# Optimization experiments

Hardware: AMD Instinct MI355X
Metric: run time of the kernel (lower is better)

## Reference

```python
import jax, jax.numpy as jnp
import numpy as np

B, T, D, H, L, F = 32, 512, 1024, 1024, 2, 256  # batch, time, input dim, units, layers, feature_size


def setup_inputs() -> dict:
    key = jax.random.key(0)
    ks = jax.random.split(key, 9)
    s_in = 1.0 / np.sqrt(D)
    s_h = 1.0 / np.sqrt(H)
    x = jax.random.normal(ks[0], (B, T, D), dtype=jnp.float32)
    # Stacked LSTM params: gate order [i, f, g, o] concatenated along last axis.
    Wx = jax.random.normal(ks[1], (L, D, 4 * H), dtype=jnp.float32) * s_in
    Wh = jax.random.normal(ks[2], (L, H, 4 * H), dtype=jnp.float32) * s_h
    b = jnp.zeros((L, 4 * H), dtype=jnp.float32)
    # Output heads.
    Wmu = jax.random.normal(ks[3], (H, F), dtype=jnp.float32) * s_h
    bmu = jnp.zeros((F,), dtype=jnp.float32)
    Wls = jax.random.normal(ks[4], (H, F), dtype=jnp.float32) * s_h
    bls = jnp.zeros((F,), dtype=jnp.float32)
    y_min = jnp.zeros((F,), dtype=jnp.float32)  # y_min init arg (0.0 broadcast)
    return {"x": x, "Wx": Wx, "Wh": Wh, "b": b, "Wmu": Wmu, "bmu": bmu,
            "Wls": Wls, "bls": bls, "y_min": y_min}


def _lstm_layer(x, Wx, Wh, b):
    # x: [B, T, Din]; Wx: [Din, 4H]; Wh: [H, 4H]; b: [4H]
    Bn = x.shape[0]
    Hn = Wh.shape[0]
    # Precompute input projections for all timesteps (one big GEMM).
    x_proj = jnp.einsum('btd,dg->btg', x, Wx) + b  # [B, T, 4H]

    def step(carry, xp):
        h, c = carry
        g = xp + h @ Wh  # [B, 4H]
        i, f, gg, o = jnp.split(g, 4, axis=-1)
        c = jax.nn.sigmoid(f) * c + jax.nn.sigmoid(i) * jnp.tanh(gg)
        h = jax.nn.sigmoid(o) * jnp.tanh(c)
        return (h, c), h

    h0 = jnp.zeros((Bn, Hn), dtype=x.dtype)
    c0 = jnp.zeros((Bn, Hn), dtype=x.dtype)
    _, hs = jax.lax.scan(step, (h0, c0), jnp.swapaxes(x_proj, 0, 1))  # hs: [T, B, H]
    return jnp.swapaxes(hs, 0, 1)  # [B, T, H]


def reference(x, Wx, Wh, b, Wmu, bmu, Wls, bls, y_min):
    for l in range(Wx.shape[0]):  # small fixed n_layers loop
        x = _lstm_layer(x, Wx[l], Wh[l], b[l])
    mu = jax.nn.softplus(x @ Wmu + bmu) + y_min  # [B, T, F]
    log_sigma = x @ Wls + bls                    # [B, T, F]
    return (mu, log_sigma)
```

## Files before the change

kernel.cpp:

```cpp
#include <hip/hip_runtime.h>

typedef unsigned short u16;
typedef unsigned int   u32;
typedef unsigned long long u64;
typedef short s16x4 __attribute__((ext_vector_type(4)));
typedef short s16x8 __attribute__((ext_vector_type(8)));
typedef float f32x4 __attribute__((ext_vector_type(4)));
typedef u32   u32x4 __attribute__((ext_vector_type(4)));

#define GK 1024

__device__ inline u16 f2bf(float f) {
    u32 u = __builtin_bit_cast(u32, f);
    u += 0x7FFFu + ((u >> 16) & 1u);
    return (u16)(u >> 16);
}
__device__ inline u16 f2h(float f) {
    _Float16 h = (_Float16)f;
    return __builtin_bit_cast(u16, h);
}
__device__ inline float h2f(u16 u) {
    return (float)__builtin_bit_cast(_Float16, u);
}
__device__ inline float fast_sigmoid(float x) {
    return __builtin_amdgcn_rcpf(1.f + __expf(-x));
}
__device__ inline float fast_tanh(float x) {
    return 1.f - 2.f * __builtin_amdgcn_rcpf(1.f + __expf(2.f * x));
}
__device__ inline f32x4 mfma16(s16x8 a, s16x8 b, f32x4 c) {
    return __builtin_amdgcn_mfma_f32_16x16x32_bf16(a, b, c, 0, 0, 0);
}
__device__ inline s16x8 mk8(s16x4 lo, s16x4 hi) {
    return __builtin_shufflevector(lo, hi, 0, 1, 2, 3, 4, 5, 6, 7);
}

__global__ void k_f2bf(const float* __restrict__ in, u16* __restrict__ out, int n) {
    int i = (blockIdx.x * 256 + threadIdx.x) * 4;
    if (i < n) {
        float4 v = *(const float4*)(in + i);
        ushort4 o;
        o.x = f2bf(v.x); o.y = f2bf(v.y); o.z = f2bf(v.z); o.w = f2bf(v.w);
        *(ushort4*)(out + i) = o;
    }
}

__global__ void k_transpose_bf(const float* __restrict__ in, u16* __restrict__ out,
                               int R, int C) {
    __shared__ float tile[32][33];
    int tid = threadIdx.x;
    int xs = (tid & 7) * 4;
    int y  = tid >> 3;
    int r0 = blockIdx.y * 32, c0 = blockIdx.x * 32;
    float4 v = *(const float4*)(in + (size_t)(r0 + y) * C + c0 + xs);
    tile[y][xs + 0] = v.x; tile[y][xs + 1] = v.y;
    tile[y][xs + 2] = v.z; tile[y][xs + 3] = v.w;
    __syncthreads();
    ushort4 o;
    o.x = f2bf(tile[xs + 0][y]); o.y = f2bf(tile[xs + 1][y]);
    o.z = f2bf(tile[xs + 2][y]); o.w = f2bf(tile[xs + 3][y]);
    *(ushort4*)(out + (size_t)(c0 + y) * R + r0 + xs) = o;
}

template<int MODE>
__launch_bounds__(256, 2)
__global__ void k_gemm(const u16* __restrict__ A, const u16* __restrict__ BT,
                       const float* __restrict__ bias,
                       u16* __restrict__ Cb, float* __restrict__ Cf,
                       const float* __restrict__ b2, const float* __restrict__ ymin,
                       int gridN) {
    int bid = blockIdx.x;
    int m0 = (bid / gridN) * 128, n0 = (bid % gridN) * 128;
    __shared__ u16 As[128 * 40];
    __shared__ u16 Bs[128 * 40];
    int tid = threadIdx.x;
    int lane = tid & 63, w = tid >> 6;
    int wr = w >> 1, wc = w & 1;
    int rr = lane & 15, r16 = lane >> 4;
    f32x4 acc[4][4] = {};
    for (int kt = 0; kt < GK / 32; ++kt) {
        int k0 = kt * 32;
#pragma unroll
        for (int it = 0; it < 2; ++it) {
            int idx = it * 256 + tid;
            int row = idx >> 2, ch = idx & 3;
            if (MODE == 0) {
                *(u32x4*)(&As[row * 40 + ch * 8]) =
                    *(const u32x4*)(A + (size_t)(m0 + row) * GK + k0 + ch * 8);
            } else {
                int m = m0 + row;
                size_t aaddr = (size_t)(m >> 5) * 32768 + (size_t)((k0 >> 3) + ch) * 256
                             + (size_t)(m & 31) * 8;
                *(u32x4*)(&As[row * 40 + ch * 8]) = *(const u32x4*)(A + aaddr);
            }
            *(u32x4*)(&Bs[row * 40 + ch * 8]) =
                *(const u32x4*)(BT + (size_t)(n0 + row) * GK + k0 + ch * 8);
        }
        __syncthreads();
        s16x8 af[4], bfr[4];
#pragma unroll
        for (int i = 0; i < 4; ++i) {
            int abase = (wr * 64 + i * 16 + rr) * 40 + r16 * 4;
            af[i] = mk8(*(const s16x4*)(&As[abase]), *(const s16x4*)(&As[abase + 16]));
            int bbase = (wc * 64 + i * 16 + rr) * 40 + r16 * 4;
            bfr[i] = mk8(*(const s16x4*)(&Bs[bbase]), *(const s16x4*)(&Bs[bbase + 16]));
        }
#pragma unroll
        for (int i = 0; i < 4; ++i)
#pragma unroll
            for (int j = 0; j < 4; ++j)
                acc[i][j] = mfma16(af[i], bfr[j], acc[i][j]);
        __syncthreads();
    }
#pragma unroll
    for (int i = 0; i < 4; ++i) {
#pragma unroll
        for (int j = 0; j < 4; ++j) {
#pragma unroll
            for (int r = 0; r < 4; ++r) {
                int m = m0 + wr * 64 + i * 16 + r16 * 4 + r;
                int n = n0 + wc * 64 + j * 16 + rr;
                float v = acc[i][j][r];
                if (MODE == 0) {
                    v += bias[n];
                    int orow = (m & 511) * 32 + (m >> 9);
                    int colx = ((n & 1023) << 2) | (n >> 10);
                    Cb[(size_t)orow * 4096 + colx] = f2h(v);
                } else {
                    int orow = (m & 31) * 512 + (m >> 5);
                    if (n < 256) {
                        v += bias[n];
                        float sp = fmaxf(v, 0.f) + log1pf(expf(-fabsf(v)));
                        Cf[(size_t)orow * 256 + n] = sp + ymin[n];
                    } else {
                        v += b2[n - 256];
                        Cf[4194304 + (size_t)orow * 256 + (n - 256)] = v;
                    }
                }
            }
        }
    }
}

__launch_bounds__(512, 2)
__global__ void k_fused(const u16* __restrict__ Wh0T, const u16* __restrict__ Wx1T,
                        const u16* __restrict__ Wh1T, const u16* __restrict__ xproj,
                        const float* __restrict__ b1,
                        u16* __restrict__ hseq0, u16* __restrict__ hseq1,
                        u32* __restrict__ flags) {
    __shared__ u16 wlds[2][32][128][8];
    __shared__ float part[4][64][4];
    int tid = threadIdx.x, blk = blockIdx.x;
    int lane = tid & 63, w = tid >> 6;
    int grp = w >> 2, wl = w & 3;
    int mt = wl >> 1, nt = wl & 1;
    int u0 = blk * 8;
    int rr = lane & 15, r16 = lane >> 4;

    int cg = (rr & 3) * 1024 + u0 + nt * 4 + (rr >> 2);
    if (wl < 2) {
        const u16* wsrc = (grp == 0 ? Wh0T : Wh1T) + (size_t)cg * GK + r16 * 4;
#pragma unroll
        for (int q = 0; q < 32; ++q) {
            s16x8 f = mk8(*(const s16x4*)(wsrc + q * 32),
                          *(const s16x4*)(wsrc + q * 32 + 16));
            *(s16x8*)(&wlds[grp][q][nt * 64 + lane][0]) = f;
        }
    }
    u64 wpx_u = (u64)(uintptr_t)(Wx1T + (size_t)cg * GK + r16 * 4);

    int b_    = mt * 16 + (lane >> 4) * 4 + (lane & 3);
    int u_loc = nt * 4 + ((lane >> 2) & 3);
    int unit  = u0 + u_loc;
    float c0 = 0.f, c1 = 0.f;
    float b1r[4];
#pragma unroll
    for (int g = 0; g < 4; ++g) b1r[g] = b1[g * 1024 + unit];

    const u16* xp = xproj + (size_t)b_ * 4096 + (size_t)unit * 4;
    const int boff = (mt * 16 + rr) * 8 + (r16 & 1) * 4;
    const int kq   = (r16 >> 1);
    const int soff = blk * 256 + b_ * 8 + nt * 4;
    const u16* wq = &wlds[grp][0][nt * 64 + lane][0];

    __syncthreads();

    for (int r = 0; r <= 512; ++r) {
        if (w == 0) {
            u32 tgt = (u32)r;
            while (true) {
                u32 v0 = __hip_atomic_load(&flags[lane], __ATOMIC_RELAXED,
                                           __HIP_MEMORY_SCOPE_AGENT);
                u32 v1 = __hip_atomic_load(&flags[64 + lane], __ATOMIC_RELAXED,
                                           __HIP_MEMORY_SCOPE_AGENT);
                if (__all((v0 >= tgt) & (v1 >= tgt))) break;
                __builtin_amdgcn_s_sleep(1);
            }
        }
        __syncthreads();

        f32x4 aE = {}, aO = {}, xE = {}, xO = {};
        u64 xv = 0;
        if (grp == 0) {
            if (r < 512) xv = *(const u64*)(xp + (size_t)r * 131072);
            asm volatile("" : "+v"(wpx_u));
            const u16* wpx = (const u16*)(uintptr_t)wpx_u;
            const u16* h0p = hseq0 + (size_t)r * 32768 + boff;
#pragma unroll
            for (int c = 0; c < 4; ++c) {
                u64 lo8[8], hi8[8];
                s16x8 bx[8];
#pragma unroll
                for (int j = 0; j < 8; ++j) {
                    int q = c * 8 + j;
                    lo8[j] = __hip_atomic_load((const u64*)(h0p + (q * 4 + kq) * 256),
                                               __ATOMIC_RELAXED, __HIP_MEMORY_SCOPE_AGENT);
                    hi8[j] = __hip_atomic_load((const u64*)(h0p + (q * 4 + kq + 2) * 256),
                                               __ATOMIC_RELAXED, __HIP_MEMORY_SCOPE_AGENT);
                    bx[j] = mk8(*(const s16x4*)(wpx + q * 32),
                                *(const s16x4*)(wpx + q * 32 + 16));
                }
#pragma unroll
                for (int j = 0; j < 8; ++j) {
                    int q = c * 8 + j;
                    s16x8 a = mk8(__builtin_bit_cast(s16x4, lo8[j]),
                                  __builtin_bit_cast(s16x4, hi8[j]));
                    s16x8 bw = *(const s16x8*)(wq + (size_t)q * 1024);
                    if (q & 1) { aO = mfma16(a, bw, aO); xO = mfma16(a, bx[j], xO); }
                    else       { aE = mfma16(a, bw, aE); xE = mfma16(a, bx[j], xE); }
                }
            }
        } else {
            if (r > 0) {
                const u16* h1p = hseq1 + (size_t)(r - 1) * 32768 + boff;
#pragma unroll
                for (int c = 0; c < 4; ++c) {
                    u64 lo8[8], hi8[8];
#pragma unroll
                    for (int j = 0; j < 8; ++j) {
                        int q = c * 8 + j;
                        lo8[j] = __hip_atomic_load((const u64*)(h1p + (q * 4 + kq) * 256),
                                                   __ATOMIC_RELAXED, __HIP_MEMORY_SCOPE_AGENT);
                        hi8[j] = __hip_atomic_load((const u64*)(h1p + (q * 4 + kq + 2) * 256),
                                                   __ATOMIC_RELAXED, __HIP_MEMORY_SCOPE_AGENT);
                    }
#pragma unroll
                    for (int j = 0; j < 8; ++j) {
                        int q = c * 8 + j;
                        s16x8 a = mk8(__builtin_bit_cast(s16x4, lo8[j]),
                                      __builtin_bit_cast(s16x4, hi8[j]));
                        s16x8 bw = *(const s16x8*)(wq + (size_t)q * 1024);
                        if (q & 1) aO = mfma16(a, bw, aO);
                        else       aE = mfma16(a, bw, aE);
                    }
                }
            }
            *(f32x4*)(&part[wl][lane][0]) = aE + aO;
        }
        __syncthreads();

        if (grp == 0) {
            if (r < 512) {
                f32x4 acc = aE + aO;
                float r0 = acc[0], r1 = acc[1], r2 = acc[2], r3 = acc[3];
                float x0 = __shfl_xor(r0, 1), x1 = __shfl_xor(r1, 1);
                float x2 = __shfl_xor(r2, 1), x3 = __shfl_xor(r3, 1);
                bool o1 = lane & 1;
                float s0 = o1 ? x1 : r0, s1 = o1 ? r1 : x0;
                float s2 = o1 ? x3 : r2, s3 = o1 ? r3 : x2;
                float y0 = __shfl_xor(s0, 2), y1 = __shfl_xor(s1, 2);
                float y2 = __shfl_xor(s2, 2), y3 = __shfl_xor(s3, 2);
                bool o2 = lane & 2;
                float gi = (o2 ? y2 : s0) + h2f((u16)(xv));
                float gf = (o2 ? y3 : s1) + h2f((u16)(xv >> 16));
                float gg = (o2 ? s2 : y0) + h2f((u16)(xv >> 32));
                float go = (o2 ? s3 : y1) + h2f((u16)(xv >> 48));
                float I  = fast_sigmoid(gi);
                float Fg = fast_sigmoid(gf);
                float G  = fast_tanh(gg);
                float O  = fast_sigmoid(go);
                c0 = Fg * c0 + I * G;
                u32 hq = (u32)f2bf(O * fast_tanh(c0));
                u32 o4 = (u32)__shfl_xor((int)hq, 4);
                u32 m32 = (lane & 4) ? ((o4 & 0xffffu) | (hq << 16))
                                     : ((hq & 0xffffu) | (o4 << 16));
                u32 o8 = (u32)__shfl_xor((int)m32, 8);
                u64 m64 = (lane & 8) ? (((u64)o8) | ((u64)m32 << 32))
                                     : (((u64)m32) | ((u64)o8 << 32));
                if ((lane & 12) == 0)
                    __hip_atomic_store((u64*)(hseq0 + (size_t)(r + 1) * 32768 + soff),
                                       m64, __ATOMIC_RELAXED, __HIP_MEMORY_SCOPE_AGENT);
            }
            if (r > 0) {
                f32x4 acc = xE + xO + *(const f32x4*)(&part[wl][lane][0]);
                float r0 = acc[0], r1 = acc[1], r2 = acc[2], r3 = acc[3];
                float x0 = __shfl_xor(r0, 1), x1 = __shfl_xor(r1, 1);
                float x2 = __shfl_xor(r2, 1), x3 = __shfl_xor(r3, 1);
                bool o1 = lane & 1;
                float s0 = o1 ? x1 : r0, s1 = o1 ? r1 : x0;
                float s2 = o1 ? x3 : r2, s3 = o1 ? r3 : x2;
                float y0 = __shfl_xor(s0, 2), y1 = __shfl_xor(s1, 2);
                float y2 = __shfl_xor(s2, 2), y3 = __shfl_xor(s3, 2);
                bool o2 = lane & 2;
                float gi = (o2 ? y2 : s0) + b1r[0];
                float gf = (o2 ? y3 : s1) + b1r[1];
                float gg = (o2 ? s2 : y0) + b1r[2];
                float go = (o2 ? s3 : y1) + b1r[3];
                float I  = fast_sigmoid(gi);
                float Fg = fast_sigmoid(gf);
                float G  = fast_tanh(gg);
                float O  = fast_sigmoid(go);
                c1 = Fg * c1 + I * G;
                u32 hq = (u32)f2bf(O * fast_tanh(c1));
                u32 o4 = (u32)__shfl_xor((int)hq, 4);
                u32 m32 = (lane & 4) ? ((o4 & 0xffffu) | (hq << 16))
                                     : ((hq & 0xffffu) | (o4 << 16));
                u32 o8 = (u32)__shfl_xor((int)m32, 8);
                u64 m64 = (lane & 8) ? (((u64)o8) | ((u64)m32 << 32))
                                     : (((u64)m32) | ((u64)o8 << 32));
                if ((lane & 12) == 0)
                    __hip_atomic_store((u64*)(hseq1 + (size_t)r * 32768 + soff),
                                       m64, __ATOMIC_RELAXED, __HIP_MEMORY_SCOPE_AGENT);
            }
        }
        __syncthreads();
        if (tid == 0)
            __hip_atomic_store(&flags[blk], (u32)(r + 1), __ATOMIC_RELAXED,
                               __HIP_MEMORY_SCOPE_AGENT);
    }
}

extern "C" void kernel_launch(void* const* d_in, const int* in_sizes, int n_in,
                              void* d_out, int out_size, void* d_ws, size_t ws_size,
                              hipStream_t stream) {
    const float* x   = (const float*)d_in[0];
    const float* Wx  = (const float*)d_in[1];
    const float* Wh  = (const float*)d_in[2];
    const float* b   = (const float*)d_in[3];
    const float* Wmu = (const float*)d_in[4];
    const float* bmu = (const float*)d_in[5];
    const float* Wls = (const float*)d_in[6];
    const float* bls = (const float*)d_in[7];
    const float* ym  = (const float*)d_in[8];
    float* out = (float*)d_out;

    char* ws = (char*)d_ws;
    u16* hseq0 = (u16*)(ws);
    u16* xbf   = (u16*)(ws);
    u16* hseq1 = (u16*)(ws + 33619968);
    u16* wxT   = (u16*)(ws + 67239936);
    u16* whT   = (u16*)(ws + 84017152);
    u16* whdT  = (u16*)(ws + 100794368);
    u16* xproj = (u16*)(ws + 101842944);
    u32* flags = (u32*)(ws + 236060672);

    k_f2bf<<<16384, 256, 0, stream>>>(x, xbf, 16777216);
    dim3 tg(128, 32);
    k_transpose_bf<<<tg, 256, 0, stream>>>(Wx,           wxT,           1024, 4096);
    k_transpose_bf<<<tg, 256, 0, stream>>>(Wx + 4194304, wxT + 4194304, 1024, 4096);
    k_transpose_bf<<<tg, 256, 0, stream>>>(Wh,           whT,           1024, 4096);
    k_transpose_bf<<<tg, 256, 0, stream>>>(Wh + 4194304, whT + 4194304, 1024, 4096);
    dim3 hg(8, 32);
    k_transpose_bf<<<hg, 256, 0, stream>>>(Wmu, whdT,          1024, 256);
    k_transpose_bf<<<hg, 256, 0, stream>>>(Wls, whdT + 262144, 1024, 256);

    k_gemm<0><<<4096, 256, 0, stream>>>(xbf, wxT, b, xproj, nullptr, nullptr, nullptr, 32);

    hipMemsetAsync(hseq0, 0, 65536, stream);
    hipMemsetAsync(hseq1, 0, 65536, stream);
    hipMemsetAsync(flags, 0, 512, stream);

    k_fused<<<128, 512, 0, stream>>>(whT, wxT + 4194304, whT + 4194304, xproj,
                                     b + 4096, hseq0, hseq1, flags);

    k_gemm<1><<<512, 256, 0, stream>>>(hseq1 + 32768, whdT, bmu, nullptr, out,
                                       bls, ym, 4);
}
```

Measured before the change: 8.023 ms.

## Split recurrent K across wave pairs and relayout hidden-state exchange buffers

Reorganizes the fused recurrent LSTM kernel so each wave pair splits the K dimension in halves and covers both N tiles, reducing partial sums through shared memory. The hidden-state sequence buffer layout changes to a contiguous per-K-chunk format, so loads become two adjacent 8-byte atomics instead of strided ones. A new unpack kernel converts the layer-1 hidden states to row-major before the head GEMM, which then drops its special addressing path. Occupancy hint is lowered to one block per CU. The aim is to shorten the per-timestep critical path, at the cost of an extra unpack pass and more LDS reduction traffic.

```diff
diff --git a/kernel.cpp b/kernel.cpp
--- a/kernel.cpp
+++ b/kernel.cpp
@@ -33,6 +33,9 @@
 }
 __device__ inline s16x8 mk8(s16x4 lo, s16x4 hi) {
     return __builtin_shufflevector(lo, hi, 0, 1, 2, 3, 4, 5, 6, 7);
+}
+__device__ inline u64 ald(const u16* p) {
+    return __hip_atomic_load((const u64*)p, __ATOMIC_RELAXED, __HIP_MEMORY_SCOPE_AGENT);
 }
 
 __global__ void k_f2bf(const float* __restrict__ in, u16* __restrict__ out, int n) {
@@ -60,6 +63,19 @@
     o.x = f2bf(tile[xs + 0][y]); o.y = f2bf(tile[xs + 1][y]);
     o.z = f2bf(tile[xs + 2][y]); o.w = f2bf(tile[xs + 3][y]);
     *(ushort4*)(out + (size_t)(c0 + y) * R + r0 + xs) = o;
+}
+
+__global__ void k_unpack(const u16* __restrict__ in, u16* __restrict__ out) {
+    int idx = blockIdx.x * 256 + threadIdx.x;
+    int slot = idx >> 12;
+    int c = idx & 4095;
+    int q = c >> 7, b = (c >> 2) & 31, ri = c & 3;
+    const u16* p = in + (size_t)(slot + 1) * 32768 + q * 1024 + b * 32 + ri * 8;
+    u64 lo = *(const u64*)p;
+    u64 hi = *(const u64*)(p + 4);
+    u16* o = out + (size_t)(slot * 32 + b) * 1024 + q * 32 + ri * 4;
+    *(u64*)o = lo;
+    *(u64*)(o + 16) = hi;
 }
 
 template<int MODE>
@@ -84,15 +100,8 @@
         for (int it = 0; it < 2; ++it) {
             int idx = it * 256 + tid;
             int row = idx >> 2, ch = idx & 3;
-            if (MODE == 0) {
-                *(u32x4*)(&As[row * 40 + ch * 8]) =
-                    *(const u32x4*)(A + (size_t)(m0 + row) * GK + k0 + ch * 8);
-            } else {
-                int m = m0 + row;
-                size_t aaddr = (size_t)(m >> 5) * 32768 + (size_t)((k0 >> 3) + ch) * 256
-                             + (size_t)(m & 31) * 8;
-                *(u32x4*)(&As[row * 40 + ch * 8]) = *(const u32x4*)(A + aaddr);
-            }
+            *(u32x4*)(&As[row * 40 + ch * 8]) =
+                *(const u32x4*)(A + (size_t)(m0 + row) * GK + k0 + ch * 8);
             *(u32x4*)(&Bs[row * 40 + ch * 8]) =
                 *(const u32x4*)(BT + (size_t)(n0 + row) * GK + k0 + ch * 8);
         }
@@ -142,46 +151,46 @@
     }
 }
 
-__launch_bounds__(512, 2)
+__launch_bounds__(512, 1)
 __global__ void k_fused(const u16* __restrict__ Wh0T, const u16* __restrict__ Wx1T,
                         const u16* __restrict__ Wh1T, const u16* __restrict__ xproj,
                         const float* __restrict__ b1,
                         u16* __restrict__ hseq0, u16* __restrict__ hseq1,
                         u32* __restrict__ flags) {
-    __shared__ u16 wlds[2][32][128][8];
-    __shared__ float part[4][64][4];
+    __shared__ u16 wlds[2][32][2][64][8];
+    __shared__ f32x4 part[2][2][4][64];
     int tid = threadIdx.x, blk = blockIdx.x;
     int lane = tid & 63, w = tid >> 6;
     int grp = w >> 2, wl = w & 3;
-    int mt = wl >> 1, nt = wl & 1;
+    int mt = wl >> 1, qh = wl & 1;
     int u0 = blk * 8;
     int rr = lane & 15, r16 = lane >> 4;
 
-    int cg = (rr & 3) * 1024 + u0 + nt * 4 + (rr >> 2);
     if (wl < 2) {
+        int ntp = wl;
+        int cg = (rr & 3) * 1024 + u0 + ntp * 4 + (rr >> 2);
         const u16* wsrc = (grp == 0 ? Wh0T : Wh1T) + (size_t)cg * GK + r16 * 4;
 #pragma unroll
         for (int q = 0; q < 32; ++q) {
-            s16x8 f = mk8(*(const s16x4*)(wsrc + q * 32),
-                          *(const s16x4*)(wsrc + q * 32 + 16));
-            *(s16x8*)(&wlds[grp][q][nt * 64 + lane][0]) = f;
-        }
-    }
-    u64 wpx_u = (u64)(uintptr_t)(Wx1T + (size_t)cg * GK + r16 * 4);
-
-    int b_    = mt * 16 + (lane >> 4) * 4 + (lane & 3);
-    int u_loc = nt * 4 + ((lane >> 2) & 3);
-    int unit  = u0 + u_loc;
+            *(s16x8*)(&wlds[grp][q][ntp][lane][0]) =
+                mk8(*(const s16x4*)(wsrc + q * 32), *(const s16x4*)(wsrc + q * 32 + 16));
+        }
+    }
+    u64 wpx_u = (u64)(uintptr_t)(Wx1T +
+        (size_t)((rr & 3) * 1024 + u0 + (rr >> 2)) * GK + r16 * 4);
+
+    int b_ = mt * 16 + (lane >> 4) * 4 + (lane & 3);
+    int uu = (lane >> 2) & 3;
+    int unit = u0 + qh * 4 + uu;
     float c0 = 0.f, c1 = 0.f;
     float b1r[4];
 #pragma unroll
     for (int g = 0; g < 4; ++g) b1r[g] = b1[g * 1024 + unit];
-
     const u16* xp = xproj + (size_t)b_ * 4096 + (size_t)unit * 4;
-    const int boff = (mt * 16 + rr) * 8 + (r16 & 1) * 4;
-    const int kq   = (r16 >> 1);
-    const int soff = blk * 256 + b_ * 8 + nt * 4;
-    const u16* wq = &wlds[grp][0][nt * 64 + lane][0];
+
+    int sblk = blk & 3;
+    const int soff = (blk >> 2) * 1024 + b_ * 32 + (((sblk & 1) * 2 + qh) * 8 + (sblk >> 1) * 4);
+    const int cbase = qh * 16384 + mt * 512 + rr * 32 + r16 * 8;
 
     __syncthreads();
 
@@ -198,70 +207,73 @@
             }
         }
         __syncthreads();
-
-        f32x4 aE = {}, aO = {}, xE = {}, xO = {};
+        __builtin_amdgcn_sched_barrier(0);
+
+        f32x4 a0[2] = {}, a1[2] = {};
         u64 xv = 0;
         if (grp == 0) {
             if (r < 512) xv = *(const u64*)(xp + (size_t)r * 131072);
             asm volatile("" : "+v"(wpx_u));
             const u16* wpx = (const u16*)(uintptr_t)wpx_u;
-            const u16* h0p = hseq0 + (size_t)r * 32768 + boff;
+            const u16* hp = hseq0 + (size_t)r * 32768 + cbase;
 #pragma unroll
             for (int c = 0; c < 4; ++c) {
-                u64 lo8[8], hi8[8];
-                s16x8 bx[8];
-#pragma unroll
-                for (int j = 0; j < 8; ++j) {
-                    int q = c * 8 + j;
-                    lo8[j] = __hip_atomic_load((const u64*)(h0p + (q * 4 + kq) * 256),
-                                               __ATOMIC_RELAXED, __HIP_MEMORY_SCOPE_AGENT);
-                    hi8[j] = __hip_atomic_load((const u64*)(h0p + (q * 4 + kq + 2) * 256),
-                                               __ATOMIC_RELAXED, __HIP_MEMORY_SCOPE_AGENT);
-                    bx[j] = mk8(*(const s16x4*)(wpx + q * 32),
-                                *(const s16x4*)(wpx + q * 32 + 16));
+                u64 lo4[4], hi4[4];
+                s16x8 bx0[4], bx1[4];
+#pragma unroll
+                for (int j = 0; j < 4; ++j) {
+                    int jj = c * 4 + j;
+                    int q = qh * 16 + jj;
+                    lo4[j] = ald(hp + jj * 1024);
+                    hi4[j] = ald(hp + jj * 1024 + 4);
+                    const u16* bp = wpx + q * 32;
+                    bx0[j] = mk8(*(const s16x4*)bp, *(const s16x4*)(bp + 16));
+                    bx1[j] = mk8(*(const s16x4*)(bp + 4096),
+                                 *(const s16x4*)(bp + 4096 + 16));
                 }
 #pragma unroll
-                for (int j = 0; j < 8; ++j) {
-                    int q = c * 8 + j;
-                    s16x8 a = mk8(__builtin_bit_cast(s16x4, lo8[j]),
-                                  __builtin_bit_cast(s16x4, hi8[j]));
-                    s16x8 bw = *(const s16x8*)(wq + (size_t)q * 1024);
-                    if (q & 1) { aO = mfma16(a, bw, aO); xO = mfma16(a, bx[j], xO); }
-                    else       { aE = mfma16(a, bw, aE); xE = mfma16(a, bx[j], xE); }
+                for (int j = 0; j < 4; ++j) {
+                    int q = qh * 16 + c * 4 + j;
+                    s16x8 a = mk8(__builtin_bit_cast(s16x4, lo4[j]),
+                                  __builtin_bit_cast(s16x4, hi4[j]));
+                    a0[0] = mfma16(a, *(const s16x8*)(&wlds[0][q][0][lane][0]), a0[0]);
+                    a0[1] = mfma16(a, *(const s16x8*)(&wlds[0][q][1][lane][0]), a0[1]);
+                    a1[0] = mfma16(a, bx0[j], a1[0]);
+                    a1[1] = mfma16(a, bx1[j], a1[1]);
                 }
             }
+            part[mt][1 - qh][0][lane] = a0[1 - qh];
+            part[mt][1 - qh][1][lane] = a1[1 - qh];
         } else {
             if (r > 0) {
-                const u16* h1p = hseq1 + (size_t)(r - 1) * 32768 + boff;
+                const u16* hp = hseq1 + (size_t)(r - 1) * 32768 + cbase;
 #pragma unroll
                 for (int c = 0; c < 4; ++c) {
-                    u64 lo8[8], hi8[8];
-#pragma unroll
-                    for (int j = 0; j < 8; ++j) {
-                        int q = c * 8 + j;
-                        lo8[j] = __hip_atomic_load((const u64*)(h1p + (q * 4 + kq) * 256),
-                                                   __ATOMIC_RELAXED, __HIP_MEMORY_SCOPE_AGENT);
-                        hi8[j] = __hip_atomic_load((const u64*)(h1p + (q * 4 + kq + 2) * 256),
-                                                   __ATOMIC_RELAXED, __HIP_MEMORY_SCOPE_AGENT);
+                    u64 lo4[4], hi4[4];
+#pragma unroll
+                    for (int j = 0; j < 4; ++j) {
+                        int jj = c * 4 + j;
+                        lo4[j] = ald(hp + jj * 1024);
+                        hi4[j] = ald(hp + jj * 1024 + 4);
                     }
 #pragma unroll
-                    for (int j = 0; j < 8; ++j) {
-                        int q = c * 8 + j;
-                        s16x8 a = mk8(__builtin_bit_cast(s16x4, lo8[j]),
-                                      __builtin_bit_cast(s16x4, hi8[j]));
-                        s16x8 bw = *(const s16x8*)(wq + (size_t)q * 1024);
-                        if (q & 1) aO = mfma16(a, bw, aO);
-                        else       aE = mfma16(a, bw, aE);
+                    for (int j = 0; j < 4; ++j) {
+                        int q = qh * 16 + c * 4 + j;
+                        s16x8 a = mk8(__builtin_bit_cast(s16x4, lo4[j]),
+                                      __builtin_bit_cast(s16x4, hi4[j]));
+                        a0[0] = mfma16(a, *(const s16x8*)(&wlds[1][q][0][lane][0]), a0[0]);
+                        a0[1] = mfma16(a, *(const s16x8*)(&wlds[1][q][1][lane][0]), a0[1]);
                     }
                 }
             }
-            *(f32x4*)(&part[wl][lane][0]) = aE + aO;
+            part[mt][0][2 + qh][lane] = a0[0];
+            part[mt][1][2 + qh][lane] = a0[1];
         }
         __syncthreads();
 
         if (grp == 0) {
             if (r < 512) {
-                f32x4 acc = aE + aO;
+                f32x4 acc = a0[qh] + part[mt][qh][0][lane];
                 float r0 = acc[0], r1 = acc[1], r2 = acc[2], r3 = acc[3];
                 float x0 = __shfl_xor(r0, 1), x1 = __shfl_xor(r1, 1);
                 float x2 = __shfl_xor(r2, 1), x3 = __shfl_xor(r3, 1);
@@ -292,7 +304,8 @@
                                        m64, __ATOMIC_RELAXED, __HIP_MEMORY_SCOPE_AGENT);
             }
             if (r > 0) {
-                f32x4 acc = xE + xO + *(const f32x4*)(&part[wl][lane][0]);
+                f32x4 acc = a1[qh] + part[mt][qh][1][lane]
+                          + part[mt][qh][2][lane] + part[mt][qh][3][lane];
                 float r0 = acc[0], r1 = acc[1], r2 = acc[2], r3 = acc[3];
                 float x0 = __shfl_xor(r0, 1), x1 = __shfl_xor(r1, 1);
                 float x2 = __shfl_xor(r2, 1), x3 = __shfl_xor(r3, 1);
@@ -352,6 +365,7 @@
     u16* whT   = (u16*)(ws + 84017152);
     u16* whdT  = (u16*)(ws + 100794368);
     u16* xproj = (u16*)(ws + 101842944);
+    u16* h1lin = xproj;
     u32* flags = (u32*)(ws + 236060672);
 
     k_f2bf<<<16384, 256, 0, stream>>>(x, xbf, 16777216);
@@ -373,6 +387,6 @@
     k_fused<<<128, 512, 0, stream>>>(whT, wxT + 4194304, whT + 4194304, xproj,
                                      b + 4096, hseq0, hseq1, flags);
 
-    k_gemm<1><<<512, 256, 0, stream>>>(hseq1 + 32768, whdT, bmu, nullptr, out,
-                                       bls, ym, 4);
-}
+    k_unpack<<<8192, 256, 0, stream>>>(hseq1, h1lin);
+    k_gemm<1><<<512, 256, 0, stream>>>(h1lin, whdT, bmu, nullptr, out, bls, ym, 4);
+}
```

Result: slower. 8.216 ms (+2.4%).
